# Kernel tuning notes

Hardware: AMD Instinct MI355X
Metric: run time of the kernel (lower is better)

Reference implementation:

```python
import jax, jax.numpy as jnp
import numpy as np

OFFS = [[0, -1], [-1, 0], [-1, -1], [0, -2], [-2, 0], [-2, -2], [0, -3], [-3, 0], [-3, -3]]
SIGMA = 1.2  # module's self.sigma; overseg_factor == 1.0 so the aff scaling is a no-op


def _gauss_kernel(sigma, truncate=4.0):
    # matches scipy/skimage gaussian: radius = int(truncate*sigma + 0.5)
    r = int(truncate * sigma + 0.5)
    t = np.arange(-r, r + 1)
    k = np.exp(-0.5 * (t / sigma) ** 2)
    return jnp.asarray(k / k.sum(), jnp.float32), r


def _blur_axis(x, k, r, axis):
    # x: [C,H,W]; skimage default mode='nearest' -> edge padding
    pad = [(0, 0)] * x.ndim
    pad[axis] = (r, r)
    xp = jnp.pad(x, pad, mode='edge')
    n = x.shape[axis]
    out = k[0] * jax.lax.slice_in_dim(xp, 0, n, axis=axis)
    for i in range(1, 2 * r + 1):
        out = out + k[i] * jax.lax.slice_in_dim(xp, i, i + n, axis=axis)
    return out


def gaussian_blur(x, sigma):
    k, r = _gauss_kernel(sigma)
    return _blur_axis(_blur_axis(x, k, r, 1), k, r, 2)


def naive_affinities(raw, offs):
    # per-offset intensity-difference affinity, normalized by its max
    affs = []
    for off in offs:
        rolled = jnp.roll(raw, (-off[0], -off[1]), axis=(-2, -1))
        d = jnp.sqrt(((raw - rolled) ** 2).sum(0))  # norm over channel dim
        affs.append(d / d.max())
    return jnp.stack(affs)  # [9,H,W]


def setup_inputs() -> dict:
    key = jax.random.key(0)
    k1, k2, k3, k4 = jax.random.split(key, 4)
    B, E, H, W = 4, 32, 512, 512
    return {
        'embeds': jax.random.normal(k1, (B, E, H, W), jnp.float32),
        'tf_embeds': jax.random.normal(k2, (B, E, H, W), jnp.float32),
        'raw': jax.random.uniform(k3, (1, 1, H, W), jnp.float32),
        'mask': jax.random.uniform(k4, (1, 9, H, W), jnp.float32),
    }


def reference(embeds, tf_embeds, raw, mask):
    r = raw[0]      # [C,H,W]
    m = mask[0]     # [9,H,W]
    affs = naive_affinities(gaussian_blur(r, SIGMA), OFFS)
    # sep_chnl scaling with overseg_factor=1.0 is identity; clamp as in torch
    affs = jnp.clip(affs, 0.0, 1.0)
    loss = jnp.zeros((), embeds.dtype)
    for i, off in enumerate(OFFS):
        rolled = jnp.roll(tf_embeds, (-off[0], -off[1]), axis=(-2, -1))
        dist = (1.0 - (embeds * rolled).sum(1)) * m[i][None]  # [B,H,W]
        a = affs[i] - affs[i].min()
        a = a / a.max()
        loss = loss + (dist * (0.5 - a)[None]).mean()
    return loss
```

## Files before the change

### kernel.cpp

```cpp
#include <hip/hip_runtime.h>
#include <math.h>

#define Hh 512
#define Ww 512
#define Bb 4
#define Ee 32
#define PLANE (Hh*Ww)
#define NOFF 9
#define BUFF 5632

#define WS_BLUR   0
#define WS_MIN    524304
#define WS_MAX    524320
#define WS_ACC    524336
#define WS_CNT    524338

__device__ __constant__ int d_OH[NOFF] = {0,-1,-1,0,-2,-2,0,-3,-3};
__device__ __constant__ int d_OW[NOFF] = {-1,0,-1,-2,0,-2,-3,0,-3};

__device__ __forceinline__ void gload_lds16(const float* g, float* l){
    __builtin_amdgcn_global_load_lds(
        (const __attribute__((address_space(1))) void*)g,
        (__attribute__((address_space(3))) void*)l, 16, 0, 0);
}

#define WAITV(n) asm volatile("s_waitcnt vmcnt(" #n ")" ::: "memory")
#define SCB()    __builtin_amdgcn_sched_barrier(0)
#define RBAR()   __builtin_amdgcn_s_barrier()

#define TS 32
#define HALO 5
__global__ __launch_bounds__(256) void k_blur(const float* __restrict__ raw,
                                              float* __restrict__ ws){
    __shared__ float sraw[TS+2*HALO][TS+2*HALO+1];
    __shared__ float shb [TS][TS+2*HALO+1];
    int tx = blockIdx.x & 15, ty = blockIdx.x >> 4;
    int r0 = ty*TS - HALO, c0 = tx*TS - HALO;

    double kd[11], s = 0.0;
    #pragma unroll
    for (int i = 0; i < 11; i++){
        double x = (double)(i - 5) / 1.2;
        kd[i] = exp(-0.5 * x * x);
        s += kd[i];
    }
    float w[11];
    #pragma unroll
    for (int i = 0; i < 11; i++) w[i] = (float)(kd[i] / s);

    for (int t = threadIdx.x; t < 42*42; t += 256){
        int rr = t / 42, cc = t - rr*42;
        int gr = min(max(r0+rr, 0), Hh-1);
        int gc = min(max(c0+cc, 0), Ww-1);
        sraw[rr][cc] = raw[gr*Ww + gc];
    }
    __syncthreads();
    for (int t = threadIdx.x; t < TS*42; t += 256){
        int rr = t / 42, cc = t - rr*42;
        float a = 0.f;
        #pragma unroll
        for (int i = 0; i < 11; i++) a += w[i] * sraw[rr+i][cc];
        shb[rr][cc] = a;
    }
    __syncthreads();
    for (int t = threadIdx.x; t < TS*TS; t += 256){
        int rr = t >> 5, cc = t & 31;
        float a = 0.f;
        #pragma unroll
        for (int i = 0; i < 11; i++) a += w[i] * shb[rr][cc+i];
        ws[WS_BLUR + (ty*TS+rr)*Ww + (tx*TS+cc)] = a;
    }
    if (blockIdx.x == 0){
        if (threadIdx.x < 16){
            ((unsigned int*)(ws + WS_MIN))[threadIdx.x] = 0x7F800000u;
            ((unsigned int*)(ws + WS_MAX))[threadIdx.x] = 0u;
        }
        if (threadIdx.x == 0){
            *(double*)(ws + WS_ACC) = 0.0;
            *(unsigned int*)(ws + WS_CNT) = 0u;
        }
    }
}

__global__ void k_minmax(float* __restrict__ ws){
    int idx = blockIdx.x * 512 + threadIdx.x;
    int h = idx >> 9, w = idx & 511;
    float bc = ws[WS_BLUR + idx];
    int lane = threadIdx.x & 63, wv = threadIdx.x >> 6;
    __shared__ float smn[8 * NOFF], smx[8 * NOFF];
    #pragma unroll
    for (int i = 0; i < NOFF; i++){
        int hn = (h + d_OH[i]) & (Hh-1);
        int wn = (w + d_OW[i]) & (Ww-1);
        float d = fabsf(bc - ws[WS_BLUR + hn * Ww + wn]);
        float mnv = d, mxv = d;
        for (int s = 32; s; s >>= 1){
            mnv = fminf(mnv, __shfl_xor(mnv, s));
            mxv = fmaxf(mxv, __shfl_xor(mxv, s));
        }
        if (lane == 0){ smn[wv * NOFF + i] = mnv; smx[wv * NOFF + i] = mxv; }
    }
    __syncthreads();
    if (threadIdx.x < NOFF){
        float mnv = smn[threadIdx.x], mxv = smx[threadIdx.x];
        for (int v = 1; v < 8; v++){
            mnv = fminf(mnv, smn[v * NOFF + threadIdx.x]);
            mxv = fmaxf(mxv, smx[v * NOFF + threadIdx.x]);
        }
        atomicMin((unsigned int*)(ws + WS_MIN) + threadIdx.x, __float_as_uint(mnv));
        atomicMax((unsigned int*)(ws + WS_MAX) + threadIdx.x, __float_as_uint(mxv));
    }
}

__global__ __launch_bounds__(512)
void k_main(const float* __restrict__ E, const float* __restrict__ T,
            const float* __restrict__ mask, float* __restrict__ ws,
            float* __restrict__ out){
    __shared__ float sL[4*BUFF];
    __shared__ float sp[8];

    int blk = blockIdx.x;
    int bb  = blk >> 7;
    int rg  = blk & 127;
    int row4 = rg << 2;

    int tid = threadIdx.x;
    int rq  = tid >> 7;
    int wq  = tid & 127;
    int wv  = tid >> 6;
    int ln  = tid & 63;
    int hr  = row4 + rq;
    int c0  = wq << 2;
    int cl  = (c0 - 4) & 511;
    int pix = hr * Ww + c0;

    const float* bl = ws + WS_BLUR;
    float tb[4][8];
    #pragma unroll
    for (int r = 0; r < 4; r++){
        int rr = (hr - r) & 511;
        float4 l4 = *(const float4*)(bl + rr*Ww + cl);
        float4 o4 = *(const float4*)(bl + rr*Ww + c0);
        tb[r][0]=l4.x; tb[r][1]=l4.y; tb[r][2]=l4.z; tb[r][3]=l4.w;
        tb[r][4]=o4.x; tb[r][5]=o4.y; tb[r][6]=o4.z; tb[r][7]=o4.w;
    }
    const unsigned int* mnb = (const unsigned int*)(ws + WS_MIN);
    const unsigned int* mxb = (const unsigned int*)(ws + WS_MAX);
    float mn[NOFF], inv[NOFF];
    #pragma unroll
    for (int i = 0; i < NOFF; i++){
        mn[i]  = __uint_as_float(mnb[i]);
        inv[i] = 1.f / (__uint_as_float(mxb[i]) - mn[i]);
    }
    float c[4][NOFF];
    float acc[4];
    #pragma unroll
    for (int j = 0; j < 4; j++){
        float bc = tb[0][4+j];
        float d[NOFF];
        d[0] = fabsf(bc - tb[0][3+j]);
        d[1] = fabsf(bc - tb[1][4+j]);
        d[2] = fabsf(bc - tb[1][3+j]);
        d[3] = fabsf(bc - tb[0][2+j]);
        d[4] = fabsf(bc - tb[2][4+j]);
        d[5] = fabsf(bc - tb[2][2+j]);
        d[6] = fabsf(bc - tb[0][1+j]);
        d[7] = fabsf(bc - tb[3][4+j]);
        d[8] = fabsf(bc - tb[3][1+j]);
        acc[j] = 0.f;
        #pragma unroll
        for (int i = 0; i < NOFF; i++){
            float a = (d[i] - mn[i]) * inv[i];
            float mv = ((const float*)(mask + i * PLANE + pix))[j];
            c[j][i] = mv * (0.5f - a);
            acc[j] += c[j][i];
        }
    }

    const float* Tbase = T + (size_t)bb * Ee * PLANE;
    const float* Ebase = E + (size_t)bb * Ee * PLANE;
    const float* gp0; const float* gp1; const float* gp2 = 0;
    int lo0, lo1, lo2 = 0;
    {
        int ch0 = wv, ch1 = wv + 8, ch2 = wv + 16;
        {
            int r = ch0 >> 1, hf = (ch0 & 1) << 8;
            gp0 = Tbase + ((row4 - 3 + r) & 511)*Ww + hf + ln*4;
            lo0 = r*512 + hf + ln*4;
        }
        if (ch1 < 14){
            int r = ch1 >> 1, hf = (ch1 & 1) << 8;
            gp1 = Tbase + ((row4 - 3 + r) & 511)*Ww + hf + ln*4;
            lo1 = r*512 + hf + ln*4;
        } else {
            int t2 = ch1 - 14, r = t2 >> 1, hf = (t2 & 1) << 8;
            gp1 = Ebase + (row4 + r)*Ww + hf + ln*4;
            lo1 = 7*512 + r*512 + hf + ln*4;
        }
        if (wv < 6){
            int t2 = ch2 - 14, r = t2 >> 1, hf = (t2 & 1) << 8;
            gp2 = Ebase + (row4 + r)*Ww + hf + ln*4;
            lo2 = 7*512 + r*512 + hf + ln*4;
        }
    }

    #define STG(bi, k) do { \
        size_t ko = (size_t)(k) * PLANE; \
        float* lb = sL + (bi)*BUFF; \
        gload_lds16(gp0 + ko, lb + lo0); \
        gload_lds16(gp1 + ko, lb + lo1); \
        if (wv < 6) gload_lds16(gp2 + ko, lb + lo2); \
    } while(0)

    #define CMPB(bi) do { \
        const float* tT = sL + (bi)*BUFF; \
        const float* tE = tT + 7*512; \
        float4 ev4 = *(const float4*)(tE + rq*512 + c0); \
        float s0, s1, s2, s3; \
        { const float* rp = tT + (3 + rq) * 512; \
          float4 l4 = *(const float4*)(rp + cl); \
          float4 o4 = *(const float4*)(rp + c0); \
          float t[8] = {l4.x,l4.y,l4.z,l4.w, o4.x,o4.y,o4.z,o4.w}; \
          s0 = c[0][0]*t[3]; s0 = fmaf(c[0][3], t[2], s0); s0 = fmaf(c[0][6], t[1], s0); \
          s1 = c[1][0]*t[4]; s1 = fmaf(c[1][3], t[3], s1); s1 = fmaf(c[1][6], t[2], s1); \
          s2 = c[2][0]*t[5]; s2 = fmaf(c[2][3], t[4], s2); s2 = fmaf(c[2][6], t[3], s2); \
          s3 = c[3][0]*t[6]; s3 = fmaf(c[3][3], t[5], s3); s3 = fmaf(c[3][6], t[4], s3); } \
        { const float* rp = tT + (2 + rq) * 512; \
          float4 l4 = *(const float4*)(rp + cl); \
          float4 o4 = *(const float4*)(rp + c0); \
          float t[8] = {l4.x,l4.y,l4.z,l4.w, o4.x,o4.y,o4.z,o4.w}; \
          s0 = fmaf(c[0][1], t[4], s0); s0 = fmaf(c[0][2], t[3], s0); \
          s1 = fmaf(c[1][1], t[5], s1); s1 = fmaf(c[1][2], t[4], s1); \
          s2 = fmaf(c[2][1], t[6], s2); s2 = fmaf(c[2][2], t[5], s2); \
          s3 = fmaf(c[3][1], t[7], s3); s3 = fmaf(c[3][2], t[6], s3); } \
        { const float* rp = tT + (1 + rq) * 512; \
          float4 l4 = *(const float4*)(rp + cl); \
          float4 o4 = *(const float4*)(rp + c0); \
          float t[8] = {l4.x,l4.y,l4.z,l4.w, o4.x,o4.y,o4.z,o4.w}; \
          s0 = fmaf(c[0][4], t[4], s0); s0 = fmaf(c[0][5], t[2], s0); \
          s1 = fmaf(c[1][4], t[5], s1); s1 = fmaf(c[1][5], t[3], s1); \
          s2 = fmaf(c[2][4], t[6], s2); s2 = fmaf(c[2][5], t[4], s2); \
          s3 = fmaf(c[3][4], t[7], s3); s3 = fmaf(c[3][5], t[5], s3); } \
        { const float* rp = tT + (0 + rq) * 512; \
          float4 l4 = *(const float4*)(rp + cl); \
          float4 o4 = *(const float4*)(rp + c0); \
          float t[8] = {l4.x,l4.y,l4.z,l4.w, o4.x,o4.y,o4.z,o4.w}; \
          s0 = fmaf(c[0][7], t[4], s0); s0 = fmaf(c[0][8], t[1], s0); \
          s1 = fmaf(c[1][7], t[5], s1); s1 = fmaf(c[1][8], t[2], s1); \
          s2 = fmaf(c[2][7], t[6], s2); s2 = fmaf(c[2][8], t[3], s2); \
          s3 = fmaf(c[3][7], t[7], s3); s3 = fmaf(c[3][8], t[4], s3); } \
        acc[0] = fmaf(-ev4.x, s0, acc[0]); \
        acc[1] = fmaf(-ev4.y, s1, acc[1]); \
        acc[2] = fmaf(-ev4.z, s2, acc[2]); \
        acc[3] = fmaf(-ev4.w, s3, acc[3]); \
    } while(0)

    WAITV(0); SCB();

    STG(0, 0);
    STG(1, 1);

    #pragma unroll 1
    for (int k = 0; k < 30; k++){
        STG((k + 2) & 3, k + 2);
        if (wv < 6) { WAITV(6); } else { WAITV(4); }
        SCB();
        RBAR();
        SCB();
        CMPB(k & 3);
    }
    if (wv < 6) { WAITV(3); } else { WAITV(2); }
    SCB();
    RBAR();
    SCB();
    CMPB(30 & 3);
    WAITV(0);
    SCB();
    RBAR();
    SCB();
    CMPB(31 & 3);

    float part = acc[0] + acc[1] + acc[2] + acc[3];
    for (int s = 32; s; s >>= 1) part += __shfl_xor(part, s);
    if (ln == 0) sp[wv] = part;
    __syncthreads();
    if (tid == 0){
        float bs = 0.f;
        #pragma unroll
        for (int v = 0; v < 8; v++) bs += sp[v];
        double* accp = (double*)(ws + WS_ACC);
        atomicAdd(accp, (double)bs);
        __threadfence();
        unsigned int done = atomicAdd((unsigned int*)(ws + WS_CNT), 1u);
        if (done == gridDim.x - 1){
            double v = atomicAdd(accp, 0.0);
            out[0] = (float)(v / (double)((size_t)Bb * PLANE));
        }
    }
}

extern "C" void kernel_launch(void* const* d_in, const int* in_sizes, int n_in,
                              void* d_out, int out_size, void* d_ws, size_t ws_size,
                              hipStream_t stream) {
    const float* embeds = (const float*)d_in[0];
    const float* tf     = (const float*)d_in[1];
    const float* raw    = (const float*)d_in[2];
    const float* mask   = (const float*)d_in[3];
    float* ws  = (float*)d_ws;
    float* out = (float*)d_out;

    k_blur  <<<256, 256, 0, stream>>>(raw, ws);
    k_minmax<<<PLANE/512, 512, 0, stream>>>(ws);
    k_main  <<<512, 512, 0, stream>>>(embeds, tf, mask, ws, out);
}
```

Before: 88.99 us.

## Split embedding channels across blocks and preload embeds into registers

The main kernel now splits the 32 embedding channels into 4 groups of 8, quadrupling the grid so more blocks run across the CUs. The embeds tile for each group is loaded straight into registers, so only the shifted tf_embeds rows are staged through shared memory. That shrinks the LDS buffer and allows a higher occupancy hint. In exchange, each block recomputes the affinity and mask coefficients, so mask is read four times. A per-group switch makes sure the mask-only term is added once. Indexing the register array with the runtime loop counter may force register spills to scratch memory.

```diff
diff --git a/kernel.cpp b/kernel.cpp
--- a/kernel.cpp
+++ b/kernel.cpp
@@ -7,7 +7,8 @@
 #define Ee 32
 #define PLANE (Hh*Ww)
 #define NOFF 9
-#define BUFF 5632
+#define EC 8
+#define BUFF 3584
 
 #define WS_BLUR   0
 #define WS_MIN    524304
@@ -112,7 +113,7 @@
     }
 }
 
-__global__ __launch_bounds__(512)
+__global__ __launch_bounds__(512, 4)
 void k_main(const float* __restrict__ E, const float* __restrict__ T,
             const float* __restrict__ mask, float* __restrict__ ws,
             float* __restrict__ out){
@@ -120,9 +121,11 @@
     __shared__ float sp[8];
 
     int blk = blockIdx.x;
-    int bb  = blk >> 7;
+    int bb  = blk >> 9;
+    int ec  = (blk >> 7) & 3;
     int rg  = blk & 127;
     int row4 = rg << 2;
+    int e0  = ec * EC;
 
     int tid = threadIdx.x;
     int rq  = tid >> 7;
@@ -154,6 +157,7 @@
     }
     float c[4][NOFF];
     float acc[4];
+    float csw = (ec == 0) ? 1.f : 0.f;
     #pragma unroll
     for (int j = 0; j < 4; j++){
         float bc = tb[0][4+j];
@@ -173,34 +177,27 @@
             float a = (d[i] - mn[i]) * inv[i];
             float mv = ((const float*)(mask + i * PLANE + pix))[j];
             c[j][i] = mv * (0.5f - a);
-            acc[j] += c[j][i];
-        }
-    }
-
-    const float* Tbase = T + (size_t)bb * Ee * PLANE;
-    const float* Ebase = E + (size_t)bb * Ee * PLANE;
-    const float* gp0; const float* gp1; const float* gp2 = 0;
-    int lo0, lo1, lo2 = 0;
+            acc[j] = fmaf(csw, c[j][i], acc[j]);
+        }
+    }
+
+    const float* Eb = E + (size_t)bb * Ee * PLANE + (size_t)e0 * PLANE + pix;
+    float4 ev[EC];
+    #pragma unroll
+    for (int i = 0; i < EC; i++)
+        ev[i] = *(const float4*)(Eb + (size_t)i * PLANE);
+
+    const float* Tbase = T + (size_t)bb * Ee * PLANE + (size_t)e0 * PLANE;
+    const float* gp0; const float* gp1 = 0;
+    int lo0, lo1 = 0;
     {
-        int ch0 = wv, ch1 = wv + 8, ch2 = wv + 16;
-        {
-            int r = ch0 >> 1, hf = (ch0 & 1) << 8;
-            gp0 = Tbase + ((row4 - 3 + r) & 511)*Ww + hf + ln*4;
-            lo0 = r*512 + hf + ln*4;
-        }
-        if (ch1 < 14){
-            int r = ch1 >> 1, hf = (ch1 & 1) << 8;
-            gp1 = Tbase + ((row4 - 3 + r) & 511)*Ww + hf + ln*4;
-            lo1 = r*512 + hf + ln*4;
-        } else {
-            int t2 = ch1 - 14, r = t2 >> 1, hf = (t2 & 1) << 8;
-            gp1 = Ebase + (row4 + r)*Ww + hf + ln*4;
-            lo1 = 7*512 + r*512 + hf + ln*4;
-        }
+        int r0c = wv >> 1, h0 = (wv & 1) << 8;
+        gp0 = Tbase + ((row4 - 3 + r0c) & 511)*Ww + h0 + ln*4;
+        lo0 = r0c*512 + h0 + ln*4;
         if (wv < 6){
-            int t2 = ch2 - 14, r = t2 >> 1, hf = (t2 & 1) << 8;
-            gp2 = Ebase + (row4 + r)*Ww + hf + ln*4;
-            lo2 = 7*512 + r*512 + hf + ln*4;
+            int r1c = (wv >> 1) + 4, h1 = (wv & 1) << 8;
+            gp1 = Tbase + ((row4 - 3 + r1c) & 511)*Ww + h1 + ln*4;
+            lo1 = r1c*512 + h1 + ln*4;
         }
     }
 
@@ -208,14 +205,11 @@
         size_t ko = (size_t)(k) * PLANE; \
         float* lb = sL + (bi)*BUFF; \
         gload_lds16(gp0 + ko, lb + lo0); \
-        gload_lds16(gp1 + ko, lb + lo1); \
-        if (wv < 6) gload_lds16(gp2 + ko, lb + lo2); \
+        if (wv < 6) gload_lds16(gp1 + ko, lb + lo1); \
     } while(0)
 
-    #define CMPB(bi) do { \
+    #define CMPB(bi, EV) do { \
         const float* tT = sL + (bi)*BUFF; \
-        const float* tE = tT + 7*512; \
-        float4 ev4 = *(const float4*)(tE + rq*512 + c0); \
         float s0, s1, s2, s3; \
         { const float* rp = tT + (3 + rq) * 512; \
           float4 l4 = *(const float4*)(rp + cl); \
@@ -249,10 +243,10 @@
           s1 = fmaf(c[1][7], t[5], s1); s1 = fmaf(c[1][8], t[2], s1); \
           s2 = fmaf(c[2][7], t[6], s2); s2 = fmaf(c[2][8], t[3], s2); \
           s3 = fmaf(c[3][7], t[7], s3); s3 = fmaf(c[3][8], t[4], s3); } \
-        acc[0] = fmaf(-ev4.x, s0, acc[0]); \
-        acc[1] = fmaf(-ev4.y, s1, acc[1]); \
-        acc[2] = fmaf(-ev4.z, s2, acc[2]); \
-        acc[3] = fmaf(-ev4.w, s3, acc[3]); \
+        acc[0] = fmaf(-(EV).x, s0, acc[0]); \
+        acc[1] = fmaf(-(EV).y, s1, acc[1]); \
+        acc[2] = fmaf(-(EV).z, s2, acc[2]); \
+        acc[3] = fmaf(-(EV).w, s3, acc[3]); \
     } while(0)
 
     WAITV(0); SCB();
@@ -261,24 +255,24 @@
     STG(1, 1);
 
     #pragma unroll 1
-    for (int k = 0; k < 30; k++){
+    for (int k = 0; k < EC-2; k++){
         STG((k + 2) & 3, k + 2);
-        if (wv < 6) { WAITV(6); } else { WAITV(4); }
+        if (wv < 6) { WAITV(4); } else { WAITV(2); }
         SCB();
         RBAR();
         SCB();
-        CMPB(k & 3);
-    }
-    if (wv < 6) { WAITV(3); } else { WAITV(2); }
+        CMPB(k & 3, ev[k]);
+    }
+    if (wv < 6) { WAITV(2); } else { WAITV(1); }
     SCB();
     RBAR();
     SCB();
-    CMPB(30 & 3);
+    CMPB((EC-2) & 3, ev[EC-2]);
     WAITV(0);
     SCB();
     RBAR();
     SCB();
-    CMPB(31 & 3);
+    CMPB((EC-1) & 3, ev[EC-1]);
 
     float part = acc[0] + acc[1] + acc[2] + acc[3];
     for (int s = 32; s; s >>= 1) part += __shfl_xor(part, s);
@@ -311,5 +305,5 @@
 
     k_blur  <<<256, 256, 0, stream>>>(raw, ws);
     k_minmax<<<PLANE/512, 512, 0, stream>>>(ws);
-    k_main  <<<512, 512, 0, stream>>>(embeds, tf, mask, ws, out);
-}
+    k_main  <<<2048, 512, 0, stream>>>(embeds, tf, mask, ws, out);
+}
```

Result: slower. 212.9 us (+139.3%).
